# Optimization experiments

Measured on AMD Instinct MI355X. Metric: run time of the kernel, lower is better.

The kernel has to match this reference:

```python
import jax, jax.numpy as jnp
import numpy as np

N, E, F_IN, D, X_DIM, T_DIM = 5000, 80000, 32, 64, 3, 6
P1, P2, H = 256, 32, 256
LOG_SCALE = 1.4763057  # sqrt(c) * 1.4763057 with c=1; Euclidean logmap0 is identity
W_DATA, W_PDE, W_ENT = 1.0, 1.0, 1.0

def time_encode(t):
    k_lin = T_DIM // 2
    k_log = T_DIM - k_lin
    s_lin = 10.0 ** jnp.arange(2, 2 * T_DIM, 1, dtype=jnp.float32)
    s_log = 10.0 ** jnp.arange(-2, 2 * T_DIM, 1, dtype=jnp.float32)
    t_lin = (t / jnp.clip(s_lin, 1e-7))[:k_lin]
    t_log = jnp.log((t / jnp.clip(s_log, 1e-7))[:k_log] + 1.0)
    return jnp.concatenate([t_lin, t_log])

def _forward(x0, adj, t, y, W_enc, W_pool1, W_pool2, W_emb1, W_emb2, W1, b1, W2, b2):
    t0 = t[0]
    # ---- encode: encoder + Euclidean log-map scaling ----
    z_x = jnp.tanh(x0 @ W_enc)                      # [N, D+X_DIM]
    z = z_x[:, :-X_DIM] * LOG_SCALE                 # [N, D]
    x_sp = 0.0 * z_x[:, -X_DIM:]                    # eps = 0 as in encode()
    t_enc = time_encode(t0)                         # [T_DIM]
    tx = jnp.concatenate([t_enc[None, :] * jnp.ones((N, 1)), x_sp], axis=-1)  # [N, T_DIM+X_DIM]
    # ---- renorm: dense adjacency scatter + DiffPool-style coarsening ----
    A = jnp.zeros((N, N), dtype=x0.dtype).at[adj[0], adj[1]].set(1.0)
    x = z
    y_cur = y                                        # [1, N]
    z_r = z
    y_r = y
    loss_ent = 0.0
    for Wp, We in ((W_pool1, W_emb1), (W_pool2, W_emb2)):
        S = jax.nn.softmax((x @ Wp) * LOG_SCALE, axis=0)        # [m, n] soft assignment
        m, n = S.shape
        ze = jnp.tanh(A @ (x @ We))                             # GNN embed at this level
        x = jnp.einsum('ij,ik->jk', S, ze) * (n / m)            # pooled features [n, D]
        y_cur = jnp.einsum('ij,ki->kj', S, y_cur) * (n / m)     # pooled targets [1, n]
        A = jnp.einsum('ji,jk,kl->il', S, A, S)                 # S^T A S -> [n, n]
        z_r = jnp.concatenate([z_r, x], axis=0)
        y_r = jnp.concatenate([y_r, y_cur], axis=-1)
        loss_ent = loss_ent + jax.scipy.special.entr(S).mean()
    M = z_r.shape[0]                                 # N + P1 + P2
    tx_all = tx[0] * jnp.ones((M, 1))                # broadcast first row -> [M, T_DIM+X_DIM]
    # ---- decoder + val_grad_lap: nested jacfwd Hessian diagonal ----
    def decode(txz):
        h = jnp.tanh(txz @ W1 + b1)
        return h @ W2 + b2                           # [1]
    def vgl(tx_i, z_i):
        def f(tx_):
            u = decode(jnp.concatenate([tx_, z_i]))
            return u, u
        def vg(tx_):
            g, u = jax.jacfwd(f, has_aux=True)(tx_)
            return g, (g, u)
        g2, (g, u) = jax.jacfwd(vg, has_aux=True)(tx_i)  # [1, d, d]
        hess = jax.vmap(jnp.diag)(g2)                     # [1, d]
        lap = hess[:, 1:].sum(1)                          # [1]
        return u, g, lap
    u, grad, lap = jax.vmap(vgl)(tx_all, z_r)        # [M,1], [M,1,d], [M,1]
    red = u.sum(-1)                                   # reduction -> [M]
    loss_data = jnp.mean(jnp.square(red - y_r[0]))
    res = grad[:, 0, 0] - lap[:, 0]                   # heat-equation residual u_t - lap
    loss_pde = jnp.mean(jnp.square(res))
    return W_DATA * loss_data + W_PDE * loss_pde + W_ENT * loss_ent

def setup_inputs():
    key = jax.random.key(0)
    ks = jax.random.split(key, 13)
    d_tx = T_DIM + X_DIM
    return {
        'x0': jax.random.normal(ks[0], (N, F_IN), dtype=jnp.float32),
        'adj': jax.random.randint(ks[1], (2, E), 0, N),
        't': jax.random.uniform(ks[2], (1,), dtype=jnp.float32) * 100.0,
        'y': jax.random.normal(ks[3], (1, N), dtype=jnp.float32),
        'W_enc': 0.2 * jax.random.normal(ks[4], (F_IN, D + X_DIM), dtype=jnp.float32),
        'W_pool1': 0.2 * jax.random.normal(ks[5], (D, P1), dtype=jnp.float32),
        'W_pool2': 0.2 * jax.random.normal(ks[6], (D, P2), dtype=jnp.float32),
        'W_emb1': 0.1 * jax.random.normal(ks[7], (D, D), dtype=jnp.float32),
        'W_emb2': 0.1 * jax.random.normal(ks[8], (D, D), dtype=jnp.float32),
        'W1': 0.1 * jax.random.normal(ks[9], (d_tx + D, H), dtype=jnp.float32),
        'b1': 0.01 * jax.random.normal(ks[10], (H,), dtype=jnp.float32),
        'W2': 0.1 * jax.random.normal(ks[11], (H, 1), dtype=jnp.float32),
        'b2': jnp.zeros((1,), dtype=jnp.float32),
    }

def reference(x0, adj, t, y, W_enc, W_pool1, W_pool2, W_emb1, W_emb2, W1, b1, W2, b2):
    return _forward(x0, adj, t, y, W_enc, W_pool1, W_pool2, W_emb1, W_emb2, W1, b1, W2, b2)
```

## Files before the change

kernel.cpp:

```cpp
#include <hip/hip_runtime.h>
#include <math.h>

#define NN 5000
#define EE 80000
#define FIN 32
#define DD 64
#define XD 3
#define TD 6
#define PP1 256
#define PP2 32
#define HH 256
#define MM (NN + PP1 + PP2)
#define CAP 64
#define CHUNKS 200
#define LOG_SCALE 1.4763057f
#define Y2SCALE (256.f / 5000.f)

#define A2CH 40
#define X2CH 79

#define ACC_OFF   0u
#define DEG_OFF   256u
#define Y2A_OFF   20256u
#define X2_OFF    21280u
#define A2_OFF    86816u
#define BM_OFF    348960u
#define ZERO_BYTES 3473960u
#define PART_OFF  348960u
#define CSTAT_OFF 758560u
#define XW2_OFF   760608u
#define S2_OFF    826144u
#define ZE2_OFF   858912u
#define X3_OFF    924448u
#define Y3_OFF    932640u
#define BUCK_OFF  3473984u
#define ZEP_OFF   4753984u
#define Z_OFF     6033984u
#define S1_OFF    7313984u
#define AS1_OFF   12433984u
#define CQ_OFF    17553984u
#define DRES_OFF  17556032u
#define PA2_OFF   17598336u
#define PX2_OFF   28084096u
#define WS_ROOMY  33261504u

__device__ __forceinline__ float bsum256(float v, float* red) {
    int t = threadIdx.x;
    red[t] = v; __syncthreads();
    #pragma unroll
    for (int o = 128; o > 0; o >>= 1) {
        if (t < o) red[t] += red[t + o];
        __syncthreads();
    }
    float r = red[0]; __syncthreads();
    return r;
}

__global__ void stage0(const float* __restrict__ x0, const float* __restrict__ Wenc,
                       float* __restrict__ z,
                       const int* __restrict__ adj, unsigned int* __restrict__ mask,
                       int* __restrict__ bucket, int* __restrict__ deg,
                       const float* __restrict__ t, const float* __restrict__ W1,
                       const float* __restrict__ b1, float* __restrict__ cq) {
    __shared__ float te[TD];
    int b = blockIdx.x;
    if (b < 1250) {
        int gid = b * 256 + threadIdx.x;
        int i = gid >> 6, j = gid & 63;
        float s = 0.f;
        #pragma unroll
        for (int k = 0; k < FIN; ++k) s = fmaf(x0[i * FIN + k], Wenc[k * (DD + XD) + j], s);
        z[i * DD + j] = tanhf(s) * LOG_SCALE;
    } else if (b < 1563) {
        int e = (b - 1250) * 256 + threadIdx.x;
        if (e < EE) {
            int i = adj[e], j = adj[EE + e];
            unsigned int key = (unsigned int)(i * NN + j);
            unsigned int bit = 1u << (key & 31u);
            unsigned int old = atomicOr(&mask[key >> 5], bit);
            if (!(old & bit)) {
                int slot = atomicAdd(&deg[i], 1);
                if (slot < CAP) bucket[i * CAP + slot] = j;
            }
        }
    } else {
        int h = threadIdx.x;
        if (h == 0) {
            float t0 = t[0];
            te[0] = t0 / 1e2f;
            te[1] = t0 / 1e3f;
            te[2] = t0 / 1e4f;
            te[3] = logf(t0 * 100.f + 1.f);
            te[4] = logf(t0 * 10.f + 1.f);
            te[5] = logf(t0 + 1.f);
        }
        __syncthreads();
        float c = b1[h];
        #pragma unroll
        for (int j = 0; j < TD; ++j) c = fmaf(te[j], W1[j * HH + h], c);
        float q = 0.f;
        #pragma unroll
        for (int j = 1; j < TD + XD; ++j) { float w = W1[j * HH + h]; q = fmaf(w, w, q); }
        cq[h] = c;
        cq[HH + h] = q;
    }
}

template<int KK, int ACT>
__global__ void mm_t(const float* __restrict__ A, int lda, const float* __restrict__ B, int ldb,
                     float* __restrict__ C, int ldc, int Mr, int Nc, float scale) {
    int gid = blockIdx.x * blockDim.x + threadIdx.x;
    if (gid >= Mr * Nc) return;
    int i = gid / Nc, j = gid - i * Nc;
    const float* a = A + i * lda;
    const float* bp = B + j;
    float s = 0.f;
    #pragma unroll
    for (int k = 0; k < KK; ++k) s = fmaf(a[k], bp[k * ldb], s);
    if (ACT) s = tanhf(s);
    C[i * ldc + j] = s * scale;
}

__global__ void gather_embed(const int* __restrict__ bucket, const int* __restrict__ deg,
                             const float* __restrict__ z, const float* __restrict__ We1,
                             float* __restrict__ zep) {
    __shared__ float zs[4][DD];
    int w = threadIdx.x >> 6, d = threadIdx.x & 63;
    int i = (blockIdx.x << 2) + w;
    int n = min(deg[i], CAP);
    const int* bk = bucket + i * CAP;
    float a0 = 0.f, a1 = 0.f, a2 = 0.f, a3 = 0.f;
    int s = 0;
    for (; s + 4 <= n; s += 4) {
        a0 += z[bk[s] * DD + d];
        a1 += z[bk[s + 1] * DD + d];
        a2 += z[bk[s + 2] * DD + d];
        a3 += z[bk[s + 3] * DD + d];
    }
    for (; s < n; ++s) a0 += z[bk[s] * DD + d];
    zs[w][d] = (a0 + a1) + (a2 + a3);
    __syncthreads();
    float acc = 0.f;
    #pragma unroll
    for (int k = 0; k < DD; ++k) acc = fmaf(zs[w][k], We1[k * DD + d], acc);
    zep[i * DD + d] = tanhf(acc);
}

__global__ void gather_as(const int* __restrict__ bucket, const int* __restrict__ deg,
                          const float* __restrict__ S1, float* __restrict__ AS1) {
    int i = blockIdx.x, c = threadIdx.x;
    int n = min(deg[i], CAP);
    const int* bk = bucket + i * CAP;
    float a0 = 0.f, a1 = 0.f, a2 = 0.f, a3 = 0.f;
    int s = 0;
    for (; s + 4 <= n; s += 4) {
        a0 += S1[bk[s] * PP1 + c];
        a1 += S1[bk[s + 1] * PP1 + c];
        a2 += S1[bk[s + 2] * PP1 + c];
        a3 += S1[bk[s + 3] * PP1 + c];
    }
    for (; s < n; ++s) a0 += S1[bk[s] * PP1 + c];
    AS1[i * PP1 + c] = (a0 + a1) + (a2 + a3);
}

__global__ void smax_part(const float* __restrict__ S, float* __restrict__ part) {
    int c = threadIdx.x, ch = blockIdx.x;
    const float* p = S + ch * 25 * PP1 + c;
    float m = -3.0e38f;
    #pragma unroll
    for (int r = 0; r < 25; ++r) m = fmaxf(m, p[r * PP1]);
    float s = 0.f;
    #pragma unroll
    for (int r = 0; r < 25; ++r) s += expf(p[r * PP1] - m);
    part[ch * 512 + c] = m;
    part[ch * 512 + 256 + c] = s;
}

__global__ void smax_finish(const float* __restrict__ part, float* __restrict__ cstat) {
    int cg = threadIdx.x >> 5, w = threadIdx.x & 31;
    int c = (blockIdx.x << 3) + cg;
    float m = -3.0e38f;
    for (int ch = w; ch < CHUNKS; ch += 32) m = fmaxf(m, part[ch * 512 + c]);
    float s = 0.f;
    for (int ch = w; ch < CHUNKS; ch += 32) s += part[ch * 512 + 256 + c] * expf(part[ch * 512 + c] - m);
    #pragma unroll
    for (int o = 16; o > 0; o >>= 1) {
        float mo = __shfl_xor(m, o);
        float so = __shfl_xor(s, o);
        float mn = fmaxf(m, mo);
        s = s * expf(m - mn) + so * expf(mo - mn);
        m = mn;
    }
    if (w == 0) cstat[c] = m + logf(s);
}

__global__ void smax_norm(float* __restrict__ S, const float* __restrict__ cstat,
                          const float* __restrict__ y, float* __restrict__ y2acc,
                          float* __restrict__ ent) {
    __shared__ float red[256];
    __shared__ float ybuf[4][64];
    int rt = blockIdx.x % 79, ct = blockIdx.x / 79;
    int lc = threadIdx.x & 63, lr = threadIdx.x >> 6;
    int c = (ct << 6) + lc;
    float mxlns = cstat[c];
    float en = 0.f, ys = 0.f;
    #pragma unroll
    for (int k = 0; k < 16; ++k) {
        int r = (rt << 6) + (k << 2) + lr;
        if (r < NN) {
            float v = S[r * PP1 + c];
            float s = expf(v - mxlns);
            S[r * PP1 + c] = s;
            en += s * (mxlns - v);
            ys = fmaf(s, y[r], ys);
        }
    }
    ybuf[lr][lc] = ys;
    en = bsum256(en, red);
    if (threadIdx.x == 0) atomicAdd(ent, en);
    if (lr == 0) atomicAdd(&y2acc[c], ybuf[0][lc] + ybuf[1][lc] + ybuf[2][lc] + ybuf[3][lc]);
}

__global__ __launch_bounds__(256) void gemm_fused(
        const float* __restrict__ S1, const float* __restrict__ AS1,
        const float* __restrict__ zep, float* __restrict__ PA2, float* __restrict__ PX2) {
    __shared__ float sa[32][64];
    __shared__ float sb[32][64];
    int b = blockIdx.x;
    const float* B;
    float* dst;
    int tm, tn, k0, k1, NB;
    if (b < 640) {
        int tile = b & 15, chunk = b >> 4;
        tm = (tile >> 2) << 6; tn = (tile & 3) << 6;
        k0 = chunk * 128; k1 = min(k0 + 128, NN);
        B = AS1; NB = PP1;
        dst = PA2 + chunk * (PP1 * PP1);
    } else {
        int b2 = b - 640;
        int tile = b2 & 3, chunk = b2 >> 2;
        tm = tile << 6; tn = 0;
        k0 = chunk * 64; k1 = min(k0 + 64, NN);
        B = zep; NB = DD;
        dst = PX2 + chunk * (PP1 * DD);
    }
    int tid = threadIdx.x;
    int tx = (tid & 15) << 2;
    int ty = (tid >> 4) << 2;
    int r0 = tid >> 4, c0 = (tid & 15) << 2;
    int r1 = (tid + 256) >> 4, c1 = c0;
    float acc[4][4] = {};
    const float4 z4 = make_float4(0.f, 0.f, 0.f, 0.f);
    for (int kb = k0; kb < k1; kb += 32) {
        int ka0 = kb + r0, ka1 = kb + r1;
        *(float4*)&sa[r0][c0] = (ka0 < k1) ? *(const float4*)&S1[ka0 * PP1 + tm + c0] : z4;
        *(float4*)&sa[r1][c1] = (ka1 < k1) ? *(const float4*)&S1[ka1 * PP1 + tm + c1] : z4;
        *(float4*)&sb[r0][c0] = (ka0 < k1) ? *(const float4*)&B[ka0 * NB + tn + c0] : z4;
        *(float4*)&sb[r1][c1] = (ka1 < k1) ? *(const float4*)&B[ka1 * NB + tn + c1] : z4;
        __syncthreads();
        #pragma unroll
        for (int kk = 0; kk < 32; ++kk) {
            float4 av = *(const float4*)&sa[kk][ty];
            float4 bv = *(const float4*)&sb[kk][tx];
            acc[0][0] = fmaf(av.x, bv.x, acc[0][0]);
            acc[0][1] = fmaf(av.x, bv.y, acc[0][1]);
            acc[0][2] = fmaf(av.x, bv.z, acc[0][2]);
            acc[0][3] = fmaf(av.x, bv.w, acc[0][3]);
            acc[1][0] = fmaf(av.y, bv.x, acc[1][0]);
            acc[1][1] = fmaf(av.y, bv.y, acc[1][1]);
            acc[1][2] = fmaf(av.y, bv.z, acc[1][2]);
            acc[1][3] = fmaf(av.y, bv.w, acc[1][3]);
            acc[2][0] = fmaf(av.z, bv.x, acc[2][0]);
            acc[2][1] = fmaf(av.z, bv.y, acc[2][1]);
            acc[2][2] = fmaf(av.z, bv.z, acc[2][2]);
            acc[2][3] = fmaf(av.z, bv.w, acc[2][3]);
            acc[3][0] = fmaf(av.w, bv.x, acc[3][0]);
            acc[3][1] = fmaf(av.w, bv.y, acc[3][1]);
            acc[3][2] = fmaf(av.w, bv.z, acc[3][2]);
            acc[3][3] = fmaf(av.w, bv.w, acc[3][3]);
        }
        __syncthreads();
    }
    #pragma unroll
    for (int i = 0; i < 4; ++i)
        *(float4*)&dst[(tm + ty + i) * NB + tn + tx] =
            make_float4(acc[i][0], acc[i][1], acc[i][2], acc[i][3]);
}

__global__ void reduce_parts(const float* __restrict__ PA2, const float* __restrict__ PX2,
                             float* __restrict__ A2, float* __restrict__ x2) {
    int idx = blockIdx.x * 256 + threadIdx.x;
    if (idx < PP1 * PP1) {
        float s = 0.f;
        #pragma unroll 8
        for (int c = 0; c < A2CH; ++c) s += PA2[c * (PP1 * PP1) + idx];
        A2[idx] = s;
    } else {
        int e = idx - PP1 * PP1;
        float s = 0.f;
        #pragma unroll 8
        for (int c = 0; c < X2CH; ++c) s += PX2[c * (PP1 * DD) + e];
        x2[e] = s * Y2SCALE;
    }
}

__global__ void gemm_tn(const float* __restrict__ A, const float* __restrict__ B,
                        float* __restrict__ C, int M, int N, int K, int kchunk, float scale) {
    __shared__ float sa[32][64];
    __shared__ float sb[32][64];
    int tilesN = N >> 6;
    int tm = (blockIdx.x / tilesN) << 6;
    int tn = (blockIdx.x % tilesN) << 6;
    int k0 = blockIdx.y * kchunk;
    int k1 = min(k0 + kchunk, K);
    int tid = threadIdx.x;
    int tx = (tid & 15) << 2;
    int ty = (tid >> 4) << 2;
    float acc[4][4] = {};
    for (int kb = k0; kb < k1; kb += 32) {
        #pragma unroll
        for (int t = 0; t < 8; ++t) {
            int idx = tid + (t << 8);
            int r = idx >> 6, cc = idx & 63;
            int k = kb + r;
            sa[r][cc] = (k < k1) ? A[k * M + tm + cc] : 0.f;
            sb[r][cc] = (k < k1) ? B[k * N + tn + cc] : 0.f;
        }
        __syncthreads();
        #pragma unroll
        for (int kk = 0; kk < 32; ++kk) {
            float4 av = *(const float4*)&sa[kk][ty];
            float4 bv = *(const float4*)&sb[kk][tx];
            acc[0][0] = fmaf(av.x, bv.x, acc[0][0]);
            acc[0][1] = fmaf(av.x, bv.y, acc[0][1]);
            acc[0][2] = fmaf(av.x, bv.z, acc[0][2]);
            acc[0][3] = fmaf(av.x, bv.w, acc[0][3]);
            acc[1][0] = fmaf(av.y, bv.x, acc[1][0]);
            acc[1][1] = fmaf(av.y, bv.y, acc[1][1]);
            acc[1][2] = fmaf(av.y, bv.z, acc[1][2]);
            acc[1][3] = fmaf(av.y, bv.w, acc[1][3]);
            acc[2][0] = fmaf(av.z, bv.x, acc[2][0]);
            acc[2][1] = fmaf(av.z, bv.y, acc[2][1]);
            acc[2][2] = fmaf(av.z, bv.z, acc[2][2]);
            acc[2][3] = fmaf(av.z, bv.w, acc[2][3]);
            acc[3][0] = fmaf(av.w, bv.x, acc[3][0]);
            acc[3][1] = fmaf(av.w, bv.y, acc[3][1]);
            acc[3][2] = fmaf(av.w, bv.z, acc[3][2]);
            acc[3][3] = fmaf(av.w, bv.w, acc[3][3]);
        }
        __syncthreads();
    }
    #pragma unroll
    for (int i = 0; i < 4; ++i)
        #pragma unroll
        for (int j = 0; j < 4; ++j)
            atomicAdd(&C[(tm + ty + i) * N + tn + tx + j], acc[i][j] * scale);
}

__global__ void mm2_fused(const float* __restrict__ x2, const float* __restrict__ We2,
                          const float* __restrict__ Wp2, float* __restrict__ XW2,
                          float* __restrict__ S2) {
    int gid = blockIdx.x * 256 + threadIdx.x;
    if (gid < PP1 * DD) {
        int i = gid >> 6, j = gid & 63;
        float s = 0.f;
        #pragma unroll
        for (int k = 0; k < DD; ++k) s = fmaf(x2[i * DD + k], We2[k * DD + j], s);
        XW2[gid] = s;
    } else {
        int e = gid - PP1 * DD;
        int i = e >> 5, j = e & 31;
        float s = 0.f;
        #pragma unroll
        for (int k = 0; k < DD; ++k) s = fmaf(x2[i * DD + k], Wp2[k * PP2 + j], s);
        S2[e] = s * LOG_SCALE;
    }
}

__global__ void level2b(float* __restrict__ S2, float* __restrict__ ent,
                        const float* __restrict__ y2acc, float* __restrict__ y3,
                        const float* __restrict__ A2, const float* __restrict__ XW2,
                        float* __restrict__ ze2) {
    __shared__ float red[256];
    int t = threadIdx.x;
    if (blockIdx.x < PP2) {
        int p = blockIdx.x;
        float l = S2[t * PP2 + p];
        red[t] = l; __syncthreads();
        #pragma unroll
        for (int o = 128; o > 0; o >>= 1) {
            if (t < o) red[t] = fmaxf(red[t], red[t + o]);
            __syncthreads();
        }
        float mx = red[0]; __syncthreads();
        float ex = expf(l - mx);
        float sum = bsum256(ex, red);
        float lns = logf(sum), inv = 1.f / sum;
        float s = ex * inv;
        S2[t * PP2 + p] = s;
        float en = s * (mx + lns - l);
        float ys = s * y2acc[t];
        en = bsum256(en, red);
        ys = bsum256(ys, red);
        if (t == 0) {
            atomicAdd(ent, en);
            y3[p] = ys * ((32.f / 256.f) * Y2SCALE);
        }
    } else {
        int gid = (blockIdx.x - PP2) * 256 + t;
        int i = gid >> 6, j = gid & 63;
        const float* a = A2 + i * PP1;
        float s = 0.f;
        #pragma unroll 16
        for (int k = 0; k < PP1; ++k) s = fmaf(a[k], XW2[k * DD + j], s);
        ze2[gid] = tanhf(s);
    }
}

__global__ void pool_x3(const float* __restrict__ S2, const float* __restrict__ ze2,
                        float* __restrict__ x3) {
    __shared__ float pr[4][64];
    int j = blockIdx.x;
    int d = threadIdx.x & 63, q = threadIdx.x >> 6;
    float a = 0.f;
    #pragma unroll 4
    for (int i = q * 64; i < q * 64 + 64; ++i)
        a = fmaf(S2[i * PP2 + j], ze2[i * DD + d], a);
    pr[q][d] = a;
    __syncthreads();
    if (q == 0) x3[j * DD + d] = (pr[0][d] + pr[1][d] + pr[2][d] + pr[3][d]) * (32.f / 256.f);
}

__global__ __launch_bounds__(256) void decoder8(
        const float* __restrict__ z, const float* __restrict__ x2,
        const float* __restrict__ x3, const float* __restrict__ y,
        const float* __restrict__ y2acc, const float* __restrict__ y3,
        const float* __restrict__ W1, const float* __restrict__ W2,
        const float* __restrict__ b2, const float* __restrict__ cq,
        float* __restrict__ dres) {
    __shared__ float zr[8][DD];
    __shared__ float rw[8][3][4];
    int t = threadIdx.x;
    int i0 = blockIdx.x << 3;
    #pragma unroll
    for (int e = t; e < 512; e += 256) {
        int r = e >> 6, d = e & 63;
        int i = i0 + r;
        float v;
        if (i < NN) v = z[i * DD + d];
        else if (i < NN + PP1) v = x2[(i - NN) * DD + d];
        else v = x3[(i - NN - PP1) * DD + d];
        zr[r][d] = v;
    }
    __syncthreads();
    int h = t;
    float c0 = cq[h];
    float a[8];
    #pragma unroll
    for (int r = 0; r < 8; ++r) a[r] = c0;
    #pragma unroll 8
    for (int k = 0; k < DD; ++k) {
        float w = W1[(TD + XD + k) * HH + h];
        #pragma unroll
        for (int r = 0; r < 8; ++r) a[r] = fmaf(zr[r][k], w, a[r]);
    }
    float w2h = W2[h], w1h = W1[h], qh = cq[HH + h];
    float pu[8], pg[8], pl[8];
    #pragma unroll
    for (int r = 0; r < 8; ++r) {
        float th = tanhf(a[r]);
        float g1 = 1.f - th * th;
        pu[r] = w2h * th;
        pg[r] = w2h * g1 * w1h;
        pl[r] = w2h * (-2.f * th * g1) * qh;
    }
    #pragma unroll
    for (int o = 32; o > 0; o >>= 1) {
        #pragma unroll
        for (int r = 0; r < 8; ++r) {
            pu[r] += __shfl_xor(pu[r], o);
            pg[r] += __shfl_xor(pg[r], o);
            pl[r] += __shfl_xor(pl[r], o);
        }
    }
    int wave = t >> 6, lane = t & 63;
    if (lane == 0) {
        #pragma unroll
        for (int r = 0; r < 8; ++r) {
            rw[r][0][wave] = pu[r];
            rw[r][1][wave] = pg[r];
            rw[r][2][wave] = pl[r];
        }
    }
    __syncthreads();
    if (t < 8) {
        int r = t, i = i0 + r;
        float su = rw[r][0][0] + rw[r][0][1] + rw[r][0][2] + rw[r][0][3];
        float sg = rw[r][1][0] + rw[r][1][1] + rw[r][1][2] + rw[r][1][3];
        float sl = rw[r][2][0] + rw[r][2][1] + rw[r][2][2] + rw[r][2][3];
        float u = su + b2[0];
        float yv = (i < NN) ? y[i]
                 : (i < NN + PP1) ? y2acc[i - NN] * Y2SCALE
                 : y3[i - NN - PP1];
        float du = u - yv;
        float res = sg - sl;
        dres[i * 2] = du * du;
        dres[i * 2 + 1] = res * res;
    }
}

__global__ void reduce_loss(const float* __restrict__ dres, const float* __restrict__ acc,
                            float* __restrict__ out) {
    __shared__ float red[256];
    int t = threadIdx.x;
    float sd = 0.f, sp = 0.f;
    for (int i = t; i < MM; i += 256) {
        sd += dres[i * 2];
        sp += dres[i * 2 + 1];
    }
    sd = bsum256(sd, red);
    sp = bsum256(sp, red);
    if (t == 0)
        out[0] = sd * (1.f / MM) + sp * (1.f / MM)
               + acc[2] * (1.f / (float)(NN * PP1)) + acc[3] * (1.f / (float)(PP1 * PP2));
}

extern "C" void kernel_launch(void* const* d_in, const int* in_sizes, int n_in,
                              void* d_out, int out_size, void* d_ws, size_t ws_size,
                              hipStream_t stream) {
    const float* x0   = (const float*)d_in[0];
    const int*   adj  = (const int*)d_in[1];
    const float* t    = (const float*)d_in[2];
    const float* y    = (const float*)d_in[3];
    const float* Wenc = (const float*)d_in[4];
    const float* Wp1  = (const float*)d_in[5];
    const float* Wp2  = (const float*)d_in[6];
    const float* We1  = (const float*)d_in[7];
    const float* We2  = (const float*)d_in[8];
    const float* W1   = (const float*)d_in[9];
    const float* b1   = (const float*)d_in[10];
    const float* W2   = (const float*)d_in[11];
    const float* b2   = (const float*)d_in[12];

    char* ws = (char*)d_ws;
    float* acc   = (float*)(ws + ACC_OFF);
    int*   deg   = (int*)(ws + DEG_OFF);
    float* y2acc = (float*)(ws + Y2A_OFF);
    float* x2    = (float*)(ws + X2_OFF);
    float* A2    = (float*)(ws + A2_OFF);
    unsigned int* mask = (unsigned int*)(ws + BM_OFF);
    float* part  = (float*)(ws + PART_OFF);
    float* cstat = (float*)(ws + CSTAT_OFF);
    float* XW2   = (float*)(ws + XW2_OFF);
    float* S2    = (float*)(ws + S2_OFF);
    float* ze2   = (float*)(ws + ZE2_OFF);
    float* x3    = (float*)(ws + X3_OFF);
    float* y3    = (float*)(ws + Y3_OFF);
    int*   buck  = (int*)(ws + BUCK_OFF);
    float* zep   = (float*)(ws + ZEP_OFF);
    float* z     = (float*)(ws + Z_OFF);
    float* S1    = (float*)(ws + S1_OFF);
    float* AS1   = (float*)(ws + AS1_OFF);
    float* cq    = (float*)(ws + CQ_OFF);
    float* dres  = (float*)(ws + DRES_OFF);
    float* PA2   = (float*)(ws + PA2_OFF);
    float* PX2   = (float*)(ws + PX2_OFF);

    hipMemsetAsync(ws, 0, ZERO_BYTES, stream);

    stage0<<<1564, 256, 0, stream>>>(x0, Wenc, z, adj, mask, buck, deg, t, W1, b1, cq);
    gather_embed<<<NN / 4, 256, 0, stream>>>(buck, deg, z, We1, zep);
    mm_t<DD, 0><<<(NN * PP1) / 256, 256, 0, stream>>>(z, DD, Wp1, PP1, S1, PP1, NN, PP1, LOG_SCALE);
    smax_part<<<CHUNKS, 256, 0, stream>>>(S1, part);
    smax_finish<<<32, 256, 0, stream>>>(part, cstat);
    smax_norm<<<79 * 4, 256, 0, stream>>>(S1, cstat, y, y2acc, &acc[2]);
    gather_as<<<NN, PP1, 0, stream>>>(buck, deg, S1, AS1);
    if (ws_size >= WS_ROOMY) {
        gemm_fused<<<640 + 316, 256, 0, stream>>>(S1, AS1, zep, PA2, PX2);
        reduce_parts<<<320, 256, 0, stream>>>(PA2, PX2, A2, x2);
    } else {
        gemm_tn<<<dim3(4, 32), 256, 0, stream>>>(S1, zep, x2, PP1, DD, NN, 157, Y2SCALE);
        gemm_tn<<<dim3(16, 16), 256, 0, stream>>>(S1, AS1, A2, PP1, PP1, NN, 313, 1.f);
    }
    mm2_fused<<<96, 256, 0, stream>>>(x2, We2, Wp2, XW2, S2);
    level2b<<<96, 256, 0, stream>>>(S2, &acc[3], y2acc, y3, A2, XW2, ze2);
    pool_x3<<<PP2, 256, 0, stream>>>(S2, ze2, x3);
    decoder8<<<MM / 8, 256, 0, stream>>>(z, x2, x3, y, y2acc, y3, W1, W2, b2, cq, dres);
    reduce_loss<<<1, 256, 0, stream>>>(dres, acc, (float*)d_out);
}
```

Before: 224.1 us.

## Fuse S1 GEMM with softmax partials, merge gather_embed, fold loss reduction into decoder

Replaces the naive per-element z@Wp1 kernel with a shared-memory tiled 64x64 GEMM that also computes per-tile column max/sum-exp partials, and runs the gather_embed work as extra blocks of the same launch. smax_part and smax_finish are removed: smax_norm now merges the 79 tile partials itself. The final reduce_loss launch is folded into decoder8 through an atomic last-block counter. stage0 stages Wenc and x0 rows in shared memory. The goal is fewer launches and less redundant global traffic, at the cost of reading partials redundantly in every smax_norm block and relying on threadfence ordering.

After: 227.4 us. About the same (+1.5%).

```diff
diff --git a/kernel.cpp b/kernel.cpp
--- a/kernel.cpp
+++ b/kernel.cpp
@@ -12,7 +12,7 @@
 #define HH 256
 #define MM (NN + PP1 + PP2)
 #define CAP 64
-#define CHUNKS 200
+#define NTILES 79
 #define LOG_SCALE 1.4763057f
 #define Y2SCALE (256.f / 5000.f)
 
@@ -20,6 +20,7 @@
 #define X2CH 79
 
 #define ACC_OFF   0u
+#define CNT_OFF   64u
 #define DEG_OFF   256u
 #define Y2A_OFF   20256u
 #define X2_OFF    21280u
@@ -27,7 +28,6 @@
 #define BM_OFF    348960u
 #define ZERO_BYTES 3473960u
 #define PART_OFF  348960u
-#define CSTAT_OFF 758560u
 #define XW2_OFF   760608u
 #define S2_OFF    826144u
 #define ZE2_OFF   858912u
@@ -56,35 +56,48 @@
     return r;
 }
 
-__global__ void stage0(const float* __restrict__ x0, const float* __restrict__ Wenc,
-                       float* __restrict__ z,
-                       const int* __restrict__ adj, unsigned int* __restrict__ mask,
-                       int* __restrict__ bucket, int* __restrict__ deg,
-                       const float* __restrict__ t, const float* __restrict__ W1,
-                       const float* __restrict__ b1, float* __restrict__ cq) {
-    __shared__ float te[TD];
+__global__ __launch_bounds__(256) void stage0(
+        const float* __restrict__ x0, const float* __restrict__ Wenc,
+        float* __restrict__ z,
+        const int* __restrict__ adj, unsigned int* __restrict__ mask,
+        int* __restrict__ bucket, int* __restrict__ deg,
+        const float* __restrict__ t, const float* __restrict__ W1,
+        const float* __restrict__ b1, float* __restrict__ cq) {
+    __shared__ float smem[FIN * DD + 4 * FIN];
     int b = blockIdx.x;
+    int tid = threadIdx.x;
     if (b < 1250) {
-        int gid = b * 256 + threadIdx.x;
-        int i = gid >> 6, j = gid & 63;
+        float (*wx)[DD] = (float(*)[DD])smem;
+        float (*xr)[FIN] = (float(*)[FIN])(smem + FIN * DD);
+        int i0 = b << 2;
+        int j = tid & 63;
+        #pragma unroll
+        for (int m = 0; m < 8; ++m) {
+            int k = (tid >> 6) + (m << 2);
+            wx[k][j] = Wenc[k * (DD + XD) + j];
+        }
+        if (tid < 128) xr[tid >> 5][tid & 31] = x0[(i0 + (tid >> 5)) * FIN + (tid & 31)];
+        __syncthreads();
+        int r = tid >> 6;
         float s = 0.f;
         #pragma unroll
-        for (int k = 0; k < FIN; ++k) s = fmaf(x0[i * FIN + k], Wenc[k * (DD + XD) + j], s);
-        z[i * DD + j] = tanhf(s) * LOG_SCALE;
+        for (int k = 0; k < FIN; ++k) s = fmaf(xr[r][k], wx[k][j], s);
+        z[(i0 + r) * DD + j] = tanhf(s) * LOG_SCALE;
     } else if (b < 1563) {
-        int e = (b - 1250) * 256 + threadIdx.x;
+        int e = (b - 1250) * 256 + tid;
         if (e < EE) {
-            int i = adj[e], j = adj[EE + e];
-            unsigned int key = (unsigned int)(i * NN + j);
+            int i = adj[e], jj = adj[EE + e];
+            unsigned int key = (unsigned int)(i * NN + jj);
             unsigned int bit = 1u << (key & 31u);
             unsigned int old = atomicOr(&mask[key >> 5], bit);
             if (!(old & bit)) {
                 int slot = atomicAdd(&deg[i], 1);
-                if (slot < CAP) bucket[i * CAP + slot] = j;
+                if (slot < CAP) bucket[i * CAP + slot] = jj;
             }
         }
     } else {
-        int h = threadIdx.x;
+        float* te = smem;
+        int h = tid;
         if (h == 0) {
             float t0 = t[0];
             te[0] = t0 / 1e2f;
@@ -97,53 +110,185 @@
         __syncthreads();
         float c = b1[h];
         #pragma unroll
-        for (int j = 0; j < TD; ++j) c = fmaf(te[j], W1[j * HH + h], c);
+        for (int j2 = 0; j2 < TD; ++j2) c = fmaf(te[j2], W1[j2 * HH + h], c);
         float q = 0.f;
         #pragma unroll
-        for (int j = 1; j < TD + XD; ++j) { float w = W1[j * HH + h]; q = fmaf(w, w, q); }
+        for (int j2 = 1; j2 < TD + XD; ++j2) { float w = W1[j2 * HH + h]; q = fmaf(w, w, q); }
         cq[h] = c;
         cq[HH + h] = q;
     }
 }
 
-template<int KK, int ACT>
-__global__ void mm_t(const float* __restrict__ A, int lda, const float* __restrict__ B, int ldb,
-                     float* __restrict__ C, int ldc, int Mr, int Nc, float scale) {
-    int gid = blockIdx.x * blockDim.x + threadIdx.x;
-    if (gid >= Mr * Nc) return;
-    int i = gid / Nc, j = gid - i * Nc;
-    const float* a = A + i * lda;
-    const float* bp = B + j;
-    float s = 0.f;
-    #pragma unroll
-    for (int k = 0; k < KK; ++k) s = fmaf(a[k], bp[k * ldb], s);
-    if (ACT) s = tanhf(s);
-    C[i * ldc + j] = s * scale;
-}
-
-__global__ void gather_embed(const int* __restrict__ bucket, const int* __restrict__ deg,
-                             const float* __restrict__ z, const float* __restrict__ We1,
-                             float* __restrict__ zep) {
-    __shared__ float zs[4][DD];
-    int w = threadIdx.x >> 6, d = threadIdx.x & 63;
-    int i = (blockIdx.x << 2) + w;
-    int n = min(deg[i], CAP);
-    const int* bk = bucket + i * CAP;
-    float a0 = 0.f, a1 = 0.f, a2 = 0.f, a3 = 0.f;
-    int s = 0;
-    for (; s + 4 <= n; s += 4) {
-        a0 += z[bk[s] * DD + d];
-        a1 += z[bk[s + 1] * DD + d];
-        a2 += z[bk[s + 2] * DD + d];
-        a3 += z[bk[s + 3] * DD + d];
-    }
-    for (; s < n; ++s) a0 += z[bk[s] * DD + d];
-    zs[w][d] = (a0 + a1) + (a2 + a3);
-    __syncthreads();
-    float acc = 0.f;
-    #pragma unroll
-    for (int k = 0; k < DD; ++k) acc = fmaf(zs[w][k], We1[k * DD + d], acc);
-    zep[i * DD + d] = tanhf(acc);
+__global__ __launch_bounds__(256) void stage1(
+        const float* __restrict__ z, const float* __restrict__ Wp1,
+        float* __restrict__ S1, float* __restrict__ part,
+        const int* __restrict__ bucket, const int* __restrict__ deg,
+        const float* __restrict__ We1, float* __restrict__ zep) {
+    __shared__ float smem[2 * 64 * 64];
+    int b = blockIdx.x;
+    int tid = threadIdx.x;
+    if (b < NTILES * 4) {
+        float (*sa)[64] = (float(*)[64])smem;
+        float (*sb)[64] = (float(*)[64])(smem + 4096);
+        int tm = (b >> 2) << 6;
+        int tn = (b & 3) << 6;
+        int r0 = tid >> 4, c0 = (tid & 15) << 2;
+        const float4 zero4 = make_float4(0.f, 0.f, 0.f, 0.f);
+        #pragma unroll
+        for (int m = 0; m < 4; ++m) {
+            int row = r0 + (m << 4);
+            int gr = tm + row;
+            *(float4*)&sa[row][c0] = (gr < NN) ? *(const float4*)&z[gr * DD + c0] : zero4;
+            *(float4*)&sb[row][c0] = *(const float4*)&Wp1[row * PP1 + tn + c0];
+        }
+        __syncthreads();
+        int tx = (tid & 15) << 2;
+        int ty = (tid >> 4) << 2;
+        float acc[4][4] = {};
+        #pragma unroll
+        for (int kk = 0; kk < 64; ++kk) {
+            float a0 = sa[ty + 0][kk];
+            float a1 = sa[ty + 1][kk];
+            float a2 = sa[ty + 2][kk];
+            float a3 = sa[ty + 3][kk];
+            float4 bv = *(const float4*)&sb[kk][tx];
+            acc[0][0] = fmaf(a0, bv.x, acc[0][0]);
+            acc[0][1] = fmaf(a0, bv.y, acc[0][1]);
+            acc[0][2] = fmaf(a0, bv.z, acc[0][2]);
+            acc[0][3] = fmaf(a0, bv.w, acc[0][3]);
+            acc[1][0] = fmaf(a1, bv.x, acc[1][0]);
+            acc[1][1] = fmaf(a1, bv.y, acc[1][1]);
+            acc[1][2] = fmaf(a1, bv.z, acc[1][2]);
+            acc[1][3] = fmaf(a1, bv.w, acc[1][3]);
+            acc[2][0] = fmaf(a2, bv.x, acc[2][0]);
+            acc[2][1] = fmaf(a2, bv.y, acc[2][1]);
+            acc[2][2] = fmaf(a2, bv.z, acc[2][2]);
+            acc[2][3] = fmaf(a2, bv.w, acc[2][3]);
+            acc[3][0] = fmaf(a3, bv.x, acc[3][0]);
+            acc[3][1] = fmaf(a3, bv.y, acc[3][1]);
+            acc[3][2] = fmaf(a3, bv.z, acc[3][2]);
+            acc[3][3] = fmaf(a3, bv.w, acc[3][3]);
+        }
+        #pragma unroll
+        for (int i2 = 0; i2 < 4; ++i2)
+            #pragma unroll
+            for (int j = 0; j < 4; ++j) acc[i2][j] *= LOG_SCALE;
+        #pragma unroll
+        for (int i2 = 0; i2 < 4; ++i2) {
+            int gr = tm + ty + i2;
+            if (gr < NN)
+                *(float4*)&S1[gr * PP1 + tn + tx] =
+                    make_float4(acc[i2][0], acc[i2][1], acc[i2][2], acc[i2][3]);
+        }
+        int nvalid = NN - (tm + ty);
+        nvalid = (nvalid < 0) ? 0 : (nvalid > 4 ? 4 : nvalid);
+        float vm[4], vs[4];
+        #pragma unroll
+        for (int j = 0; j < 4; ++j) {
+            float m = -3.0e38f;
+            #pragma unroll
+            for (int i2 = 0; i2 < 4; ++i2) if (i2 < nvalid) m = fmaxf(m, acc[i2][j]);
+            float s = 0.f;
+            #pragma unroll
+            for (int i2 = 0; i2 < 4; ++i2) if (i2 < nvalid) s += expf(acc[i2][j] - m);
+            vm[j] = m; vs[j] = s;
+        }
+        __syncthreads();
+        float* redm = smem;
+        float* reds = smem + 1024;
+        int g = tid >> 4;
+        #pragma unroll
+        for (int j = 0; j < 4; ++j) {
+            redm[g * 64 + tx + j] = vm[j];
+            reds[g * 64 + tx + j] = vs[j];
+        }
+        __syncthreads();
+        if (tid < 64) {
+            float M = -3.0e38f, S = 0.f;
+            #pragma unroll
+            for (int g2 = 0; g2 < 16; ++g2) {
+                float m2 = redm[g2 * 64 + tid], s2 = reds[g2 * 64 + tid];
+                float Mn = fmaxf(M, m2);
+                S = S * expf(M - Mn) + s2 * expf(m2 - Mn);
+                M = Mn;
+            }
+            int rt = tm >> 6;
+            part[rt * 512 + tn + tid] = M;
+            part[rt * 512 + 256 + tn + tid] = S;
+        }
+    } else {
+        float (*zs)[DD] = (float(*)[DD])smem;
+        int w = tid >> 6, d = tid & 63;
+        int i = ((b - NTILES * 4) << 2) + w;
+        int n = min(deg[i], CAP);
+        const int* bk = bucket + i * CAP;
+        float a0 = 0.f, a1 = 0.f, a2 = 0.f, a3 = 0.f;
+        int s = 0;
+        for (; s + 4 <= n; s += 4) {
+            a0 += z[bk[s] * DD + d];
+            a1 += z[bk[s + 1] * DD + d];
+            a2 += z[bk[s + 2] * DD + d];
+            a3 += z[bk[s + 3] * DD + d];
+        }
+        for (; s < n; ++s) a0 += z[bk[s] * DD + d];
+        zs[w][d] = (a0 + a1) + (a2 + a3);
+        __syncthreads();
+        float acc = 0.f;
+        #pragma unroll
+        for (int k = 0; k < DD; ++k) acc = fmaf(zs[w][k], We1[k * DD + d], acc);
+        zep[i * DD + d] = tanhf(acc);
+    }
+}
+
+__global__ void smax_norm(float* __restrict__ S, const float* __restrict__ part,
+                          const float* __restrict__ y, float* __restrict__ y2acc,
+                          float* __restrict__ ent) {
+    __shared__ float red[256];
+    __shared__ float ybuf[4][64];
+    __shared__ float cst[64];
+    int rt = blockIdx.x % NTILES, ct = blockIdx.x / NTILES;
+    int lc = threadIdx.x & 63, q = threadIdx.x >> 6;
+    int c = (ct << 6) + lc;
+    float M = -3.0e38f, Sv = 0.f;
+    for (int ch = q; ch < NTILES; ch += 4) {
+        float m2 = part[ch * 512 + c];
+        float s2 = part[ch * 512 + 256 + c];
+        float Mn = fmaxf(M, m2);
+        Sv = Sv * expf(M - Mn) + s2 * expf(m2 - Mn);
+        M = Mn;
+    }
+    red[threadIdx.x] = M; ybuf[q][lc] = Sv;
+    __syncthreads();
+    if (q == 0) {
+        float Mm = red[lc], Ss = ybuf[0][lc];
+        #pragma unroll
+        for (int g = 1; g < 4; ++g) {
+            float m2 = red[g * 64 + lc], s2 = ybuf[g][lc];
+            float Mn = fmaxf(Mm, m2);
+            Ss = Ss * expf(Mm - Mn) + s2 * expf(m2 - Mn);
+            Mm = Mn;
+        }
+        cst[lc] = Mm + logf(Ss);
+    }
+    __syncthreads();
+    float mxlns = cst[lc];
+    float en = 0.f, ys = 0.f;
+    #pragma unroll
+    for (int k = 0; k < 16; ++k) {
+        int r = (rt << 6) + (k << 2) + q;
+        if (r < NN) {
+            float v = S[r * PP1 + c];
+            float s = expf(v - mxlns);
+            S[r * PP1 + c] = s;
+            en += s * (mxlns - v);
+            ys = fmaf(s, y[r], ys);
+        }
+    }
+    __syncthreads();
+    ybuf[q][lc] = ys;
+    en = bsum256(en, red);
+    if (threadIdx.x == 0) atomicAdd(ent, en);
+    if (q == 0) atomicAdd(&y2acc[c], ybuf[0][lc] + ybuf[1][lc] + ybuf[2][lc] + ybuf[3][lc]);
 }
 
 __global__ void gather_as(const int* __restrict__ bucket, const int* __restrict__ deg,
@@ -161,64 +306,6 @@
     }
     for (; s < n; ++s) a0 += S1[bk[s] * PP1 + c];
     AS1[i * PP1 + c] = (a0 + a1) + (a2 + a3);
-}
-
-__global__ void smax_part(const float* __restrict__ S, float* __restrict__ part) {
-    int c = threadIdx.x, ch = blockIdx.x;
-    const float* p = S + ch * 25 * PP1 + c;
-    float m = -3.0e38f;
-    #pragma unroll
-    for (int r = 0; r < 25; ++r) m = fmaxf(m, p[r * PP1]);
-    float s = 0.f;
-    #pragma unroll
-    for (int r = 0; r < 25; ++r) s += expf(p[r * PP1] - m);
-    part[ch * 512 + c] = m;
-    part[ch * 512 + 256 + c] = s;
-}
-
-__global__ void smax_finish(const float* __restrict__ part, float* __restrict__ cstat) {
-    int cg = threadIdx.x >> 5, w = threadIdx.x & 31;
-    int c = (blockIdx.x << 3) + cg;
-    float m = -3.0e38f;
-    for (int ch = w; ch < CHUNKS; ch += 32) m = fmaxf(m, part[ch * 512 + c]);
-    float s = 0.f;
-    for (int ch = w; ch < CHUNKS; ch += 32) s += part[ch * 512 + 256 + c] * expf(part[ch * 512 + c] - m);
-    #pragma unroll
-    for (int o = 16; o > 0; o >>= 1) {
-        float mo = __shfl_xor(m, o);
-        float so = __shfl_xor(s, o);
-        float mn = fmaxf(m, mo);
-        s = s * expf(m - mn) + so * expf(mo - mn);
-        m = mn;
-    }
-    if (w == 0) cstat[c] = m + logf(s);
-}
-
-__global__ void smax_norm(float* __restrict__ S, const float* __restrict__ cstat,
-                          const float* __restrict__ y, float* __restrict__ y2acc,
-                          float* __restrict__ ent) {
-    __shared__ float red[256];
-    __shared__ float ybuf[4][64];
-    int rt = blockIdx.x % 79, ct = blockIdx.x / 79;
-    int lc = threadIdx.x & 63, lr = threadIdx.x >> 6;
-    int c = (ct << 6) + lc;
-    float mxlns = cstat[c];
-    float en = 0.f, ys = 0.f;
-    #pragma unroll
-    for (int k = 0; k < 16; ++k) {
-        int r = (rt << 6) + (k << 2) + lr;
-        if (r < NN) {
-            float v = S[r * PP1 + c];
-            float s = expf(v - mxlns);
-            S[r * PP1 + c] = s;
-            en += s * (mxlns - v);
-            ys = fmaf(s, y[r], ys);
-        }
-    }
-    ybuf[lr][lc] = ys;
-    en = bsum256(en, red);
-    if (threadIdx.x == 0) atomicAdd(ent, en);
-    if (lr == 0) atomicAdd(&y2acc[c], ybuf[0][lc] + ybuf[1][lc] + ybuf[2][lc] + ybuf[3][lc]);
 }
 
 __global__ __launch_bounds__(256) void gemm_fused(
@@ -437,9 +524,11 @@
         const float* __restrict__ y2acc, const float* __restrict__ y3,
         const float* __restrict__ W1, const float* __restrict__ W2,
         const float* __restrict__ b2, const float* __restrict__ cq,
-        float* __restrict__ dres) {
+        float* __restrict__ dres, int* __restrict__ cnt,
+        const float* __restrict__ acc, float* __restrict__ out) {
     __shared__ float zr[8][DD];
     __shared__ float rw[8][3][4];
+    __shared__ int lastflag;
     int t = threadIdx.x;
     int i0 = blockIdx.x << 3;
     #pragma unroll
@@ -506,23 +595,25 @@
         float res = sg - sl;
         dres[i * 2] = du * du;
         dres[i * 2 + 1] = res * res;
-    }
-}
-
-__global__ void reduce_loss(const float* __restrict__ dres, const float* __restrict__ acc,
-                            float* __restrict__ out) {
-    __shared__ float red[256];
-    int t = threadIdx.x;
-    float sd = 0.f, sp = 0.f;
-    for (int i = t; i < MM; i += 256) {
-        sd += dres[i * 2];
-        sp += dres[i * 2 + 1];
-    }
-    sd = bsum256(sd, red);
-    sp = bsum256(sp, red);
-    if (t == 0)
-        out[0] = sd * (1.f / MM) + sp * (1.f / MM)
-               + acc[2] * (1.f / (float)(NN * PP1)) + acc[3] * (1.f / (float)(PP1 * PP2));
+        __threadfence();
+    }
+    __syncthreads();
+    if (t == 0) lastflag = atomicAdd(cnt, 1);
+    __syncthreads();
+    if (lastflag == (MM / 8) - 1) {
+        __threadfence();
+        float* red = (float*)zr;
+        float sd = 0.f, sp = 0.f;
+        for (int i = t; i < MM; i += 256) {
+            sd += dres[i * 2];
+            sp += dres[i * 2 + 1];
+        }
+        sd = bsum256(sd, red);
+        sp = bsum256(sp, red);
+        if (t == 0)
+            out[0] = sd * (1.f / MM) + sp * (1.f / MM)
+                   + acc[2] * (1.f / (float)(NN * PP1)) + acc[3] * (1.f / (float)(PP1 * PP2));
+    }
 }
 
 extern "C" void kernel_launch(void* const* d_in, const int* in_sizes, int n_in,
@@ -544,13 +635,13 @@
 
     char* ws = (char*)d_ws;
     float* acc   = (float*)(ws + ACC_OFF);
+    int*   cnt   = (int*)(ws + CNT_OFF);
     int*   deg   = (int*)(ws + DEG_OFF);
     float* y2acc = (float*)(ws + Y2A_OFF);
     float* x2    = (float*)(ws + X2_OFF);
     float* A2    = (float*)(ws + A2_OFF);
     unsigned int* mask = (unsigned int*)(ws + BM_OFF);
     float* part  = (float*)(ws + PART_OFF);
-    float* cstat = (float*)(ws + CSTAT_OFF);
     float* XW2   = (float*)(ws + XW2_OFF);
     float* S2    = (float*)(ws + S2_OFF);
     float* ze2   = (float*)(ws + ZE2_OFF);
@@ -569,11 +660,8 @@
     hipMemsetAsync(ws, 0, ZERO_BYTES, stream);
 
     stage0<<<1564, 256, 0, stream>>>(x0, Wenc, z, adj, mask, buck, deg, t, W1, b1, cq);
-    gather_embed<<<NN / 4, 256, 0, stream>>>(buck, deg, z, We1, zep);
-    mm_t<DD, 0><<<(NN * PP1) / 256, 256, 0, stream>>>(z, DD, Wp1, PP1, S1, PP1, NN, PP1, LOG_SCALE);
-    smax_part<<<CHUNKS, 256, 0, stream>>>(S1, part);
-    smax_finish<<<32, 256, 0, stream>>>(part, cstat);
-    smax_norm<<<79 * 4, 256, 0, stream>>>(S1, cstat, y, y2acc, &acc[2]);
+    stage1<<<NTILES * 4 + NN / 4, 256, 0, stream>>>(z, Wp1, S1, part, buck, deg, We1, zep);
+    smax_norm<<<NTILES * 4, 256, 0, stream>>>(S1, part, y, y2acc, &acc[2]);
     gather_as<<<NN, PP1, 0, stream>>>(buck, deg, S1, AS1);
     if (ws_size >= WS_ROOMY) {
         gemm_fused<<<640 + 316, 256, 0, stream>>>(S1, AS1, zep, PA2, PX2);
@@ -585,6 +673,6 @@
     mm2_fused<<<96, 256, 0, stream>>>(x2, We2, Wp2, XW2, S2);
     level2b<<<96, 256, 0, stream>>>(S2, &acc[3], y2acc, y3, A2, XW2, ze2);
     pool_x3<<<PP2, 256, 0, stream>>>(S2, ze2, x3);
-    decoder8<<<MM / 8, 256, 0, stream>>>(z, x2, x3, y, y2acc, y3, W1, W2, b2, cq, dres);
-    reduce_loss<<<1, 256, 0, stream>>>(dres, acc, (float*)d_out);
-}
+    decoder8<<<MM / 8, 256, 0, stream>>>(z, x2, x3, y, y2acc, y3, W1, W2, b2, cq,
+                                         dres, cnt, acc, (float*)d_out);
+}
```
